# Kernel tuning notes

Hardware: AMD Instinct MI355X
Metric: run time of the kernel (lower is better)

## Reference

```python
import jax, jax.numpy as jnp
import numpy as np

C = 64
C2 = C // 2

def setup_inputs() -> dict:
    key = jax.random.key(0)
    ks = jax.random.split(key, 5)
    x = jax.random.normal(ks[0], (8, C, 64, 64), dtype=jnp.float32)
    # 1x1 conv weights stored as [out, in] matrices (kernel size 1)
    g_w = jax.random.normal(ks[1], (C2, C), dtype=jnp.float32) * (1.0 / np.sqrt(C))
    g_b = jax.random.normal(ks[2], (C2,), dtype=jnp.float32) * 0.01
    W_w = jax.random.normal(ks[3], (C, C2), dtype=jnp.float32) * (1.0 / np.sqrt(C2))
    W_b = jax.random.normal(ks[4], (C,), dtype=jnp.float32) * 0.01
    return {"x": x, "g_w": g_w, "g_b": g_b, "W_w": W_w, "W_b": W_b}

def reference(x, g_w, g_b, W_w, W_b):
    b, c, h, w = x.shape
    xf = x.reshape(b, c, h * w)                      # [B, C, N]
    # g: 1x1 conv -> [B, N, C2]
    g_x = jnp.einsum('oc,bcn->bno', g_w, xf) + g_b
    # attention scores on raw x (theta/phi convs unused in original forward)
    f = jnp.einsum('bcn,bcm->bnm', xf, xf)           # [B, N, N]
    f_div_C = jax.nn.softmax(f, axis=-1)
    y = jnp.einsum('bnm,bmo->bno', f_div_C, g_x)     # [B, N, C2]
    # W: 1x1 conv back to C channels, then residual
    W_y = jnp.einsum('co,bno->bcn', W_w, y) + W_b[None, :, None]
    z = W_y.reshape(b, c, h, w) + x
    return z
```

## Files before the change

### kernel.cpp

```cpp
#include <hip/hip_runtime.h>
#include <hip/hip_bf16.h>

#define BATCH 8
#define CH    64
#define CH2   32
#define NN    4096
#define BN    (BATCH * NN)
#define KPAD  72
#define YPAD  36
#define RPAD  40

typedef __attribute__((ext_vector_type(8)))  short        short8;
typedef __attribute__((ext_vector_type(4)))  float        floatx4;
typedef __attribute__((ext_vector_type(16))) float        floatx16;
typedef __attribute__((ext_vector_type(4)))  unsigned int uint4v;
typedef __attribute__((ext_vector_type(8)))  unsigned short ushort8v;
typedef unsigned short ushort_t;

#define LOG2E      1.4426950408889634f
#define SQRT_LOG2E 1.2011224087864498f

__device__ __forceinline__ unsigned short f2bf_rne(float f) {
    unsigned int u = __float_as_uint(f);
    return (unsigned short)((u + 0x7FFFu + ((u >> 16) & 1u)) >> 16);
}

__global__ __launch_bounds__(256) void prep_fused(const float* __restrict__ x,
                                                  const float* __restrict__ gw,
                                                  const float* __restrict__ gb,
                                                  ushort_t* __restrict__ xT,
                                                  float* __restrict__ mlog,
                                                  ushort_t* __restrict__ gxT) {
    __shared__ float gwl[CH2 * CH];
    __shared__ float gbl[CH2];
    int t = threadIdx.x;
    for (int i = t; i < CH2 * CH; i += 256) gwl[i] = gw[i];
    if (t < CH2) gbl[t] = gb[t];
    __syncthreads();

    int g   = blockIdx.x * 256 + t;
    int row = g >> 2;
    int q4  = g & 3;
    int b = row >> 12, n = row & (NN - 1);
    const float* xp = x + (size_t)b * CH * NN + n;

    float xv[16];
    float ns = 0.f;
    short8 v0, v1;
    #pragma unroll
    for (int j = 0; j < 8; ++j) {
        float a = xp[(size_t)(q4 * 16 + j) * NN];
        xv[j] = a; ns += a * a;
        v0[j] = (short)f2bf_rne(a * SQRT_LOG2E);
    }
    #pragma unroll
    for (int j = 0; j < 8; ++j) {
        float a = xp[(size_t)(q4 * 16 + 8 + j) * NN];
        xv[8 + j] = a; ns += a * a;
        v1[j] = (short)f2bf_rne(a * SQRT_LOG2E);
    }
    *(short8*)(xT + (size_t)row * CH + q4 * 16)     = v0;
    *(short8*)(xT + (size_t)row * CH + q4 * 16 + 8) = v1;
    ns += __shfl_xor(ns, 1);
    ns += __shfl_xor(ns, 2);
    if (q4 == 0) mlog[row] = 12.0f * sqrtf(ns) * LOG2E;

    float acc[CH2];
    #pragma unroll
    for (int o = 0; o < CH2; ++o) acc[o] = 0.f;
    #pragma unroll
    for (int j = 0; j < 16; ++j) {
        float a = xv[j];
        const float* gc = gwl + q4 * 16 + j;
        #pragma unroll
        for (int o = 0; o < CH2; ++o) acc[o] = fmaf(gc[o * CH], a, acc[o]);
    }
    #pragma unroll
    for (int o = 0; o < CH2; ++o) {
        acc[o] += __shfl_xor(acc[o], 1);
        acc[o] += __shfl_xor(acc[o], 2);
    }
    #pragma unroll
    for (int i = 0; i < 8; ++i) {
        int o = q4 * 8 + i;
        gxT[((size_t)b * CH2 + o) * NN + n] = f2bf_rne(acc[o] + gbl[o]);
    }
}

__global__ __launch_bounds__(256, 4) void flash_attn(const ushort_t* __restrict__ xT,
                                                     const ushort_t* __restrict__ gxT,
                                                     const float* __restrict__ mlog,
                                                     ushort_t* __restrict__ py,
                                                     float* __restrict__ pl,
                                                     int ksplit) {
    __shared__ __align__(16) unsigned char smem[4 * 32 * YPAD * 4];
    ushort_t* Klds = (ushort_t*)smem;

    const int tid = threadIdx.x, wave = tid >> 6, lane = tid & 63;
    const int q5 = lane & 31;
    const int h  = lane >> 5;
    const int bq = blockIdx.x & 255;
    const int sp = blockIdx.x >> 8;
    const int b = bq >> 5, qt = bq & 31;
    const int n0 = qt * 128 + wave * 32;
    const int k0 = sp * ksplit;

    short8 qf[4];
    {
        const ushort_t* qp = xT + ((size_t)(b * NN + n0 + q5)) * CH + h * 8;
        #pragma unroll
        for (int f = 0; f < 4; ++f) qf[f] = *(const short8*)(qp + f * 16);
    }
    const float ml = mlog[(size_t)b * NN + n0 + q5];

    short8 ones;
    #pragma unroll
    for (int j = 0; j < 8; ++j) ones[j] = (short)0x3F80;

    floatx16 yt, lt;
    #pragma unroll
    for (int i = 0; i < 16; ++i) { yt[i] = 0.f; lt[i] = 0.f; }

    const ushort_t* kb = xT + (size_t)(b * NN + k0) * CH;
    const ushort_t* vb = gxT + (size_t)b * CH2 * NN + k0;
    const int iters = ksplit >> 6;
    const int skey = tid >> 3, sc0 = (tid & 7) * 8;

    for (int kt = 0; kt < iters; ++kt) {
        short8 kv0 = *(const short8*)(kb + ((size_t)kt << 12) + (size_t)skey * CH + sc0);
        short8 kv1 = *(const short8*)(kb + ((size_t)kt << 12) + (size_t)(skey + 32) * CH + sc0);
        short8 vf[4];
        #pragma unroll
        for (int fr = 0; fr < 4; ++fr)
            vf[fr] = *(const short8*)(vb + (size_t)q5 * NN + kt * 64 + fr * 16 + h * 8);

        __syncthreads();
        *(short8*)(&Klds[skey * KPAD + sc0])        = kv0;
        *(short8*)(&Klds[(skey + 32) * KPAD + sc0]) = kv1;
        __syncthreads();

        #pragma unroll
        for (int T = 0; T < 2; ++T) {
            floatx16 st;
            #pragma unroll
            for (int i = 0; i < 16; ++i) st[i] = -ml;
            #pragma unroll
            for (int f = 0; f < 4; ++f) {
                short8 kf = *(const short8*)(&Klds[(T * 32 + q5) * KPAD + f * 16 + h * 8]);
                st = __builtin_amdgcn_mfma_f32_32x32x16_bf16(kf, qf[f], st, 0, 0, 0);
            }
            unsigned int d[8];
            #pragma unroll
            for (int r2 = 0; r2 < 8; ++r2) {
                float p0 = __builtin_amdgcn_exp2f(st[2 * r2]);
                float p1 = __builtin_amdgcn_exp2f(st[2 * r2 + 1]);
                unsigned int u0 = __float_as_uint(p0) + 0x8000u;
                unsigned int u1 = __float_as_uint(p1) + 0x8000u;
                d[r2] = __builtin_amdgcn_perm(u1, u0, 0x07060302u);
            }
            #pragma unroll
            for (int fp = 0; fp < 2; ++fp) {
                unsigned int d0 = d[fp * 4 + 0], d1 = d[fp * 4 + 1];
                unsigned int d2 = d[fp * 4 + 2], d3 = d[fp * 4 + 3];
                unsigned int e0 = (unsigned int)__shfl_xor((int)d0, 32);
                unsigned int e1 = (unsigned int)__shfl_xor((int)d1, 32);
                unsigned int e2 = (unsigned int)__shfl_xor((int)d2, 32);
                unsigned int e3 = (unsigned int)__shfl_xor((int)d3, 32);
                uint4v bv;
                bv[0] = h ? e2 : d0;
                bv[1] = h ? e3 : d1;
                bv[2] = h ? d2 : e0;
                bv[3] = h ? d3 : e1;
                short8 pb = __builtin_bit_cast(short8, bv);
                yt = __builtin_amdgcn_mfma_f32_32x32x16_bf16(vf[T * 2 + fp], pb, yt, 0, 0, 0);
                lt = __builtin_amdgcn_mfma_f32_32x32x16_bf16(ones, pb, lt, 0, 0, 0);
            }
        }
    }

    __syncthreads();
    float* yb = (float*)smem + wave * 32 * YPAD;
    #pragma unroll
    for (int reg = 0; reg < 16; ++reg) {
        int o = (reg & 3) + 8 * (reg >> 2) + 4 * h;
        yb[q5 * YPAD + o] = yt[reg];
    }
    __syncthreads();
    {
        int qq = lane >> 1, half = lane & 1;
        const float* src = yb + qq * YPAD + half * 16;
        float4 s0 = *(const float4*)(src);
        float4 s1 = *(const float4*)(src + 4);
        float4 s2 = *(const float4*)(src + 8);
        float4 s3 = *(const float4*)(src + 12);
        ushort8v pk0, pk1;
        pk0[0] = f2bf_rne(s0.x); pk0[1] = f2bf_rne(s0.y);
        pk0[2] = f2bf_rne(s0.z); pk0[3] = f2bf_rne(s0.w);
        pk0[4] = f2bf_rne(s1.x); pk0[5] = f2bf_rne(s1.y);
        pk0[6] = f2bf_rne(s1.z); pk0[7] = f2bf_rne(s1.w);
        pk1[0] = f2bf_rne(s2.x); pk1[1] = f2bf_rne(s2.y);
        pk1[2] = f2bf_rne(s2.z); pk1[3] = f2bf_rne(s2.w);
        pk1[4] = f2bf_rne(s3.x); pk1[5] = f2bf_rne(s3.y);
        pk1[6] = f2bf_rne(s3.z); pk1[7] = f2bf_rne(s3.w);
        ushort_t* dst = py + ((size_t)sp * BN + (size_t)b * NN + n0 + qq) * CH2 + half * 16;
        *(ushort8v*)(dst)     = pk0;
        *(ushort8v*)(dst + 8) = pk1;
    }
    if (h == 0) pl[(size_t)sp * BN + (size_t)b * NN + n0 + q5] = lt[0];
}

__global__ __launch_bounds__(256) void reduce_proj(const ushort_t* __restrict__ py,
                                                   const float* __restrict__ pl,
                                                   const float* __restrict__ Ww,
                                                   const float* __restrict__ Wb,
                                                   const float* __restrict__ x,
                                                   float* __restrict__ out,
                                                   int nsplit) {
    __shared__ ushort_t WwB[CH * RPAD];
    __shared__ ushort_t Y[64 * RPAD];
    __shared__ float    linv[64];
    __shared__ float    WbL[CH];

    const int t = threadIdx.x;
    const int row = t >> 2, o8 = (t & 3) * 8;
    const int grow0 = blockIdx.x * 64;

    {
        const float* wp = Ww + row * CH2 + o8;
        ushort8v w;
        #pragma unroll
        for (int j = 0; j < 8; ++j) w[j] = f2bf_rne(wp[j]);
        *(ushort8v*)(&WwB[row * RPAD + o8]) = w;
    }
    if (t < CH) WbL[t] = Wb[t];
    if (t < 64) {
        float l = 0.f;
        for (int s = 0; s < nsplit; ++s) l += pl[(size_t)s * BN + grow0 + t];
        linv[t] = 1.0f / l;
    }

    float acc[8];
    #pragma unroll
    for (int j = 0; j < 8; ++j) acc[j] = 0.f;
    for (int s = 0; s < nsplit; ++s) {
        ushort8v v = *(const ushort8v*)(py + ((size_t)s * BN + grow0 + row) * CH2 + o8);
        #pragma unroll
        for (int j = 0; j < 8; ++j)
            acc[j] += __uint_as_float((unsigned int)v[j] << 16);
    }
    __syncthreads();
    {
        float inv = linv[row];
        ushort8v yv;
        #pragma unroll
        for (int j = 0; j < 8; ++j) yv[j] = f2bf_rne(acc[j] * inv);
        *(ushort8v*)(&Y[row * RPAD + o8]) = yv;
    }
    __syncthreads();

    const int wave = t >> 6, lane = t & 63;
    const int ql = lane & 15, quad = lane >> 4;
    const int b = grow0 >> 12;
    const int nbase = (grow0 & (NN - 1)) + wave * 16;

    short8 bfrag = *(const short8*)(&Y[(wave * 16 + ql) * RPAD + quad * 8]);
    #pragma unroll
    for (int ct = 0; ct < 4; ++ct) {
        short8 afrag = *(const short8*)(&WwB[(ct * 16 + ql) * RPAD + quad * 8]);
        floatx4 d = (floatx4){0.f, 0.f, 0.f, 0.f};
        d = __builtin_amdgcn_mfma_f32_16x16x32_bf16(afrag, bfrag, d, 0, 0, 0);
        #pragma unroll
        for (int r = 0; r < 4; ++r) {
            int c = ct * 16 + quad * 4 + r;
            size_t oi = ((size_t)b * CH + c) * NN + nbase + ql;
            out[oi] = d[r] + WbL[c] + x[oi];
        }
    }
}

extern "C" void kernel_launch(void* const* d_in, const int* in_sizes, int n_in,
                              void* d_out, int out_size, void* d_ws, size_t ws_size,
                              hipStream_t stream) {
    const float* x  = (const float*)d_in[0];
    const float* gw = (const float*)d_in[1];
    const float* gb = (const float*)d_in[2];
    const float* Ww = (const float*)d_in[3];
    const float* Wb = (const float*)d_in[4];
    float* out = (float*)d_out;

    ushort_t* xT   = (ushort_t*)d_ws;
    ushort_t* gxT  = xT + (size_t)BN * CH;
    float*    mlog = (float*)(gxT + (size_t)BATCH * CH2 * NN);
    ushort_t* py   = (ushort_t*)(mlog + BN);
    size_t base_bytes = (size_t)BN * CH * 2 + (size_t)BATCH * CH2 * NN * 2 + (size_t)BN * 4;
    int split = 4;
    while (split > 1 && base_bytes + (size_t)split * BN * (CH2 * 2 + 4) > ws_size)
        split >>= 1;
    float* pl = (float*)(py + (size_t)split * BN * CH2);

    hipLaunchKernelGGL(prep_fused,  dim3(BN * 4 / 256), dim3(256), 0, stream,
                       x, gw, gb, xT, mlog, gxT);
    hipLaunchKernelGGL(flash_attn,  dim3(256 * split),  dim3(256), 0, stream,
                       xT, gxT, mlog, py, pl, NN / split);
    hipLaunchKernelGGL(reduce_proj, dim3(BN / 64),      dim3(256), 0, stream,
                       py, pl, Ww, Wb, x, out, split);
}
```

Baseline: 122.4 us.

## Double-buffer K/V tiles in LDS with prefetch and MFMA priority hints

The flash attention loop now double-buffers both the key tile and the value tile in shared memory. It prefetches the next tile into registers while computing the current one, which cuts the loop from two barriers per iteration to one. V fragments are read from LDS instead of strided global loads, and s_setprio raises wave priority around the MFMA sections. The prep kernel is reorganised to load all x values first and use row-wise float4 weight reads, and the final kernel unrolls the split-reduction loads assuming nsplit is at most 4. This adds LDS usage and a hard cap of 4 splits, which could hurt occupancy or silently drop splits beyond 4.

Measured after the change: 120.0 us. Within noise of the previous version (-1.9%).

```diff
diff --git a/kernel.cpp b/kernel.cpp
--- a/kernel.cpp
+++ b/kernel.cpp
@@ -7,8 +7,10 @@
 #define NN    4096
 #define BN    (BATCH * NN)
 #define KPAD  72
+#define VPAD  72
 #define YPAD  36
 #define RPAD  40
+#define BUFE  (64 * KPAD + 32 * VPAD)
 
 typedef __attribute__((ext_vector_type(8)))  short        short8;
 typedef __attribute__((ext_vector_type(4)))  float        floatx4;
@@ -45,19 +47,20 @@
     const float* xp = x + (size_t)b * CH * NN + n;
 
     float xv[16];
+    #pragma unroll
+    for (int j = 0; j < 16; ++j) xv[j] = xp[(size_t)(q4 * 16 + j) * NN];
+
     float ns = 0.f;
     short8 v0, v1;
     #pragma unroll
     for (int j = 0; j < 8; ++j) {
-        float a = xp[(size_t)(q4 * 16 + j) * NN];
-        xv[j] = a; ns += a * a;
-        v0[j] = (short)f2bf_rne(a * SQRT_LOG2E);
+        ns += xv[j] * xv[j];
+        v0[j] = (short)f2bf_rne(xv[j] * SQRT_LOG2E);
     }
     #pragma unroll
     for (int j = 0; j < 8; ++j) {
-        float a = xp[(size_t)(q4 * 16 + 8 + j) * NN];
-        xv[8 + j] = a; ns += a * a;
-        v1[j] = (short)f2bf_rne(a * SQRT_LOG2E);
+        ns += xv[8 + j] * xv[8 + j];
+        v1[j] = (short)f2bf_rne(xv[8 + j] * SQRT_LOG2E);
     }
     *(short8*)(xT + (size_t)row * CH + q4 * 16)     = v0;
     *(short8*)(xT + (size_t)row * CH + q4 * 16 + 8) = v1;
@@ -67,13 +70,15 @@
 
     float acc[CH2];
     #pragma unroll
-    for (int o = 0; o < CH2; ++o) acc[o] = 0.f;
-    #pragma unroll
-    for (int j = 0; j < 16; ++j) {
-        float a = xv[j];
-        const float* gc = gwl + q4 * 16 + j;
-        #pragma unroll
-        for (int o = 0; o < CH2; ++o) acc[o] = fmaf(gc[o * CH], a, acc[o]);
+    for (int o = 0; o < CH2; ++o) {
+        const float4* wr = (const float4*)(gwl + o * CH + q4 * 16);
+        float4 w0 = wr[0], w1 = wr[1], w2 = wr[2], w3 = wr[3];
+        float a;
+        a  = w0.x * xv[0]  + w0.y * xv[1]  + w0.z * xv[2]  + w0.w * xv[3];
+        a += w1.x * xv[4]  + w1.y * xv[5]  + w1.z * xv[6]  + w1.w * xv[7];
+        a += w2.x * xv[8]  + w2.y * xv[9]  + w2.z * xv[10] + w2.w * xv[11];
+        a += w3.x * xv[12] + w3.y * xv[13] + w3.z * xv[14] + w3.w * xv[15];
+        acc[o] = a;
     }
     #pragma unroll
     for (int o = 0; o < CH2; ++o) {
@@ -93,8 +98,9 @@
                                                      ushort_t* __restrict__ py,
                                                      float* __restrict__ pl,
                                                      int ksplit) {
-    __shared__ __align__(16) unsigned char smem[4 * 32 * YPAD * 4];
-    ushort_t* Klds = (ushort_t*)smem;
+    __shared__ __align__(16) ushort_t smem[2 * BUFE];
+    ushort_t* Kbase = smem;
+    ushort_t* Vbase = smem + 64 * KPAD;
 
     const int tid = threadIdx.x, wave = tid >> 6, lane = tid & 63;
     const int q5 = lane & 31;
@@ -126,29 +132,43 @@
     const int iters = ksplit >> 6;
     const int skey = tid >> 3, sc0 = (tid & 7) * 8;
 
+    {
+        short8 k0r = *(const short8*)(kb + (size_t)skey * CH + sc0);
+        short8 k1r = *(const short8*)(kb + (size_t)(skey + 32) * CH + sc0);
+        short8 v0r = *(const short8*)(vb + (size_t)skey * NN + sc0);
+        *(short8*)(&Kbase[skey * KPAD + sc0])        = k0r;
+        *(short8*)(&Kbase[(skey + 32) * KPAD + sc0]) = k1r;
+        *(short8*)(&Vbase[skey * VPAD + sc0])        = v0r;
+    }
+    __syncthreads();
+
     for (int kt = 0; kt < iters; ++kt) {
-        short8 kv0 = *(const short8*)(kb + ((size_t)kt << 12) + (size_t)skey * CH + sc0);
-        short8 kv1 = *(const short8*)(kb + ((size_t)kt << 12) + (size_t)(skey + 32) * CH + sc0);
+        const int kp = (kt + 1 < iters) ? (kt + 1) : kt;
+        const size_t kof = (size_t)kp << 12;
+        short8 nk0 = *(const short8*)(kb + kof + (size_t)skey * CH + sc0);
+        short8 nk1 = *(const short8*)(kb + kof + (size_t)(skey + 32) * CH + sc0);
+        short8 nv  = *(const short8*)(vb + (size_t)skey * NN + kp * 64 + sc0);
+
+        const ushort_t* Kl = Kbase + (kt & 1) * BUFE;
+        const ushort_t* Vl = Vbase + (kt & 1) * BUFE;
+
         short8 vf[4];
         #pragma unroll
         for (int fr = 0; fr < 4; ++fr)
-            vf[fr] = *(const short8*)(vb + (size_t)q5 * NN + kt * 64 + fr * 16 + h * 8);
-
-        __syncthreads();
-        *(short8*)(&Klds[skey * KPAD + sc0])        = kv0;
-        *(short8*)(&Klds[(skey + 32) * KPAD + sc0]) = kv1;
-        __syncthreads();
+            vf[fr] = *(const short8*)(&Vl[q5 * VPAD + fr * 16 + h * 8]);
 
         #pragma unroll
         for (int T = 0; T < 2; ++T) {
             floatx16 st;
             #pragma unroll
             for (int i = 0; i < 16; ++i) st[i] = -ml;
+            __builtin_amdgcn_s_setprio(1);
             #pragma unroll
             for (int f = 0; f < 4; ++f) {
-                short8 kf = *(const short8*)(&Klds[(T * 32 + q5) * KPAD + f * 16 + h * 8]);
+                short8 kf = *(const short8*)(&Kl[(T * 32 + q5) * KPAD + f * 16 + h * 8]);
                 st = __builtin_amdgcn_mfma_f32_32x32x16_bf16(kf, qf[f], st, 0, 0, 0);
             }
+            __builtin_amdgcn_s_setprio(0);
             unsigned int d[8];
             #pragma unroll
             for (int r2 = 0; r2 < 8; ++r2) {
@@ -172,10 +192,21 @@
                 bv[2] = h ? d2 : e0;
                 bv[3] = h ? d3 : e1;
                 short8 pb = __builtin_bit_cast(short8, bv);
+                __builtin_amdgcn_s_setprio(1);
                 yt = __builtin_amdgcn_mfma_f32_32x32x16_bf16(vf[T * 2 + fp], pb, yt, 0, 0, 0);
                 lt = __builtin_amdgcn_mfma_f32_32x32x16_bf16(ones, pb, lt, 0, 0, 0);
+                __builtin_amdgcn_s_setprio(0);
             }
         }
+
+        {
+            ushort_t* Kn = Kbase + ((kt & 1) ^ 1) * BUFE;
+            ushort_t* Vn = Vbase + ((kt & 1) ^ 1) * BUFE;
+            *(short8*)(&Kn[skey * KPAD + sc0])        = nk0;
+            *(short8*)(&Kn[(skey + 32) * KPAD + sc0]) = nk1;
+            *(short8*)(&Vn[skey * VPAD + sc0])        = nv;
+        }
+        __syncthreads();
     }
 
     __syncthreads();
@@ -234,19 +265,36 @@
     }
     if (t < CH) WbL[t] = Wb[t];
     if (t < 64) {
+        const float* plp = pl + grow0 + t;
+        float lv[4];
+        #pragma unroll
+        for (int s = 0; s < 4; ++s) {
+            int sc = s < nsplit ? s : 0;
+            lv[s] = plp[(size_t)sc * BN];
+        }
         float l = 0.f;
-        for (int s = 0; s < nsplit; ++s) l += pl[(size_t)s * BN + grow0 + t];
+        #pragma unroll
+        for (int s = 0; s < 4; ++s) if (s < nsplit) l += lv[s];
         linv[t] = 1.0f / l;
     }
 
     float acc[8];
     #pragma unroll
     for (int j = 0; j < 8; ++j) acc[j] = 0.f;
-    for (int s = 0; s < nsplit; ++s) {
-        ushort8v v = *(const ushort8v*)(py + ((size_t)s * BN + grow0 + row) * CH2 + o8);
-        #pragma unroll
-        for (int j = 0; j < 8; ++j)
-            acc[j] += __uint_as_float((unsigned int)v[j] << 16);
+    {
+        const ushort_t* pp = py + ((size_t)(grow0 + row)) * CH2 + o8;
+        ushort8v pv[4];
+        #pragma unroll
+        for (int s = 0; s < 4; ++s) {
+            int sc = s < nsplit ? s : 0;
+            pv[s] = *(const ushort8v*)(pp + (size_t)sc * BN * CH2);
+        }
+        #pragma unroll
+        for (int s = 0; s < 4; ++s) if (s < nsplit) {
+            #pragma unroll
+            for (int j = 0; j < 8; ++j)
+                acc[j] += __uint_as_float((unsigned int)pv[s][j] << 16);
+        }
     }
     __syncthreads();
     {
```
